# Optimization experiments

Measured on AMD Instinct MI355X. Metric: run time of the kernel, lower is better.

## Reference

```python
import jax, jax.numpy as jnp
import numpy as np

B, N, E, K, DI, DO = 16, 1024, 16, 3, 32, 32


def setup_inputs() -> dict:
    key = jax.random.key(0)
    k1, k2, k3, k4, k5 = jax.random.split(key, 5)
    return {
        "x": jax.random.normal(k1, (B, N, DI), dtype=jnp.float32),
        "all_emb": jax.random.normal(k2, (B, N, E), dtype=jnp.float32),
        "stock_emb": jax.random.normal(k3, (B, N, E), dtype=jnp.float32),
        "weights_pool": jax.random.normal(k4, (E, K, DI, DO), dtype=jnp.float32) * 0.1,
        "bias_pool": jax.random.normal(k5, (E, DO), dtype=jnp.float32) * 0.1,
    }


def reference(x, all_emb, stock_emb, weights_pool, bias_pool):
    # dynamic adjacency: relu(E E^T) then row softmax -> [B, N, N]
    A = jax.nn.relu(jnp.einsum('bne,bme->bnm', all_emb, all_emb))
    S = jax.nn.softmax(A, axis=-1)
    b, n, _ = S.shape
    k_orders = weights_pool.shape[1]
    eye = jnp.broadcast_to(jnp.eye(n, dtype=S.dtype), S.shape)
    # Chebyshev recursion T_0 = I, T_1 = S, T_k = 2 S T_{k-1} - T_{k-2}
    supports = [eye, S]
    for _ in range(2, k_orders):
        supports.append(2.0 * jnp.matmul(S, supports[-1]) - supports[-2])
    cheby = jnp.stack(supports, axis=1)  # [B, K, N, N]
    # graph propagation per Chebyshev order: [B, K, N, dim_in]
    x_g = jnp.einsum('bkij,bjd->bkid', cheby, x)
    # node-specific weights from stock_emb, fused with conv (avoids [B,N,K,I,O]):
    # original: weights = einsum('bni,ikop->bnkop'); out = einsum('bkni,bnkio->bnko').sum(k)
    out = jnp.einsum('bkni,bne,ekio->bno', x_g, stock_emb, weights_pool)
    bias = jnp.einsum('bne,eo->bno', stock_emb, bias_pool)
    return out + bias
```

## Files before the change

kernel.cpp:

```cpp
#include <hip/hip_runtime.h>
#include <stdint.h>

typedef __bf16 bf16x8 __attribute__((ext_vector_type(8)));
typedef __bf16 bf16x4 __attribute__((ext_vector_type(4)));
typedef float  f32x16 __attribute__((ext_vector_type(16)));

constexpr int kB = 16;
constexpr int kN = 1024;

struct bfhl { __bf16 h, l; };
__device__ __forceinline__ bfhl hilo(float v) {
    bfhl r;
    r.h = (__bf16)v;
    r.l = (__bf16)(v - (float)r.h);
    return r;
}

__device__ __forceinline__ int moff(int f, int h, int j) {
    return 16 * f + ((j < 4) ? (4 * h + j) : (4 * h + j + 4));
}


__global__ __launch_bounds__(256) void prep(
    const float* __restrict__ emb, const float* __restrict__ x,
    const float* __restrict__ Wp,
    __bf16* __restrict__ esf, __bf16* __restrict__ vtf1,
    __bf16* __restrict__ xgf, __bf16* __restrict__ wq)
{
    __shared__ float ls[64 * 36];
    const int tid = threadIdx.x;
    const int bid = blockIdx.x;

    if (bid < 256) {
        const int b = bid >> 4, rg = (bid & 15) << 6;
        const int r = tid >> 2, seg = tid & 3;
        float4 v = *(const float4*)(emb + ((size_t)(b * kN + rg + r) * 16 + seg * 4));
        float f[4] = {v.x, v.y, v.z, v.w};
        bf16x4 hi, lo;
        #pragma unroll
        for (int i = 0; i < 4; ++i) { bfhl t = hilo(f[i]); hi[i] = t.h; lo[i] = t.l; }
        const int kt = ((bid & 15) << 1) + (r >> 5);
        const int lane = ((seg >> 1) << 5) + (r & 31);
        const int j0 = (seg & 1) << 2;
        __bf16* base = esf + ((size_t)(b * 32 + kt) * 2) * 512 + lane * 8 + j0;
        *(bf16x4*)base         = hi;
        *(bf16x4*)(base + 512) = lo;
    } else if (bid < 512) {
        const int bb = bid - 256;
        const int b = bb >> 4, n0 = (bb & 15) << 6;
        const float* sB = x + ((size_t)b * kN + n0) * 32;
        #pragma unroll
        for (int it = 0; it < 2; ++it) {
            int f = it * 256 + tid;
            int row = f >> 3, q8 = f & 7;
            float4 v = *(const float4*)(sB + (size_t)row * 32 + q8 * 4);
            *(float4*)(&ls[row * 36 + q8 * 4]) = v;
        }
        __syncthreads();
        {
            const int mt = tid >> 7, fr = (tid >> 6) & 1, l = tid & 63;
            const int d = l & 31, h = l >> 5;
            bf16x8 ov;
            #pragma unroll
            for (int j = 0; j < 8; ++j)
                ov[j] = (__bf16)ls[(mt * 32 + moff(fr, h, j)) * 36 + d];
            *(bf16x8*)(vtf1 + ((size_t)(b * 32 + (n0 >> 5) + mt) * 2 + fr) * 512 + l * 8) = ov;
        }
        #pragma unroll
        for (int mt = 0; mt < 2; ++mt) {
            const int ks = tid >> 7, pl = (tid >> 6) & 1, l = tid & 63;
            const int node = l & 31, h = l >> 5;
            const float* rp = &ls[(mt * 32 + node) * 36 + ks * 16 + 8 * h];
            float4 u0 = *(const float4*)rp;
            float4 u1 = *(const float4*)(rp + 4);
            float u[8] = {u0.x, u0.y, u0.z, u0.w, u1.x, u1.y, u1.z, u1.w};
            bf16x8 ov;
            #pragma unroll
            for (int j = 0; j < 8; ++j) {
                bfhl t = hilo(u[j]);
                ov[j] = pl ? t.l : t.h;
            }
            const int ntile = b * 32 + (n0 >> 5) + mt;
            *(bf16x8*)(xgf + ((size_t)(ntile * 4 + ks) * 2 + pl) * 512 + l * 8) = ov;
        }
    } else {
        int idx = (bid - 512) * 256 + tid;
        if (idx < 6144) {
            int e = idx / 384, rem = idx - e * 384;
            int ks = rem / 64, r2 = rem - ks * 64;
            int o = r2 >> 1, h = r2 & 1;
            int ki0 = ks * 16 + h * 8;
            bf16x8 hi;
            #pragma unroll
            for (int j = 0; j < 8; ++j)
                hi[j] = (__bf16)Wp[(size_t)e * 3072 + (size_t)(ki0 + j) * 32 + o];
            *(bf16x8*)(wq + (size_t)(e * 6 + ks) * 512 + o * 16 + h * 8) = hi;
        }
    }
}

template<int STAGE>
__global__ __launch_bounds__(256, 2) void apply_mfma(
    const __bf16* __restrict__ esf,
    const __bf16* __restrict__ vtin,
    const float*  __restrict__ x,
    __bf16* __restrict__ vtout,
    __bf16* __restrict__ xgf,
    const __bf16* __restrict__ wq,
    const float*  __restrict__ stock,
    const float*  __restrict__ bias,
    float* __restrict__ out)
{
    __shared__ alignas(16) char smem[24576];
    float*  ps  = (float*)smem;
    float*  Ls  = (float*)(smem + 16896);
    float*  yb  = (float*)(smem + 17408);
    __bf16* xg2 = (__bf16*)(smem + 17408);
    float*  s_s = (float*)(smem + 22016);

    const int tid = threadIdx.x;
    const int w = tid >> 6, l = tid & 63;
    const int q = l & 31, h = l >> 5;
    const int b = blockIdx.x >> 5, q0 = (blockIdx.x & 31) << 5;
    const int ntile = blockIdx.x;

    const __bf16* esfB = esf + (size_t)b * 32768;
    const __bf16* vtfB = vtin + (size_t)b * 32768;

    if (STAGE == 2) {
        int r = tid >> 3, e2 = (tid & 7) * 2;
        *(float2*)(s_s + r * 16 + e2) =
            *(const float2*)(stock + (size_t)(b * kN + q0 + r) * 16 + e2);
    }

    bf16x8 bhi = *(const bf16x8*)(esfB + ((size_t)(q0 >> 5) * 2) * 512 + l * 8);
    bf16x8 blo = *(const bf16x8*)(esfB + ((size_t)(q0 >> 5) * 2 + 1) * 512 + l * 8);

    f32x16 acc = {};
    float Lp = 0.f;

    #pragma unroll 2
    for (int it = 0; it < 8; ++it) {
        const int kt = it * 4 + w;
        bf16x8 ahi = *(const bf16x8*)(esfB + ((size_t)kt * 2) * 512 + l * 8);
        bf16x8 alo = *(const bf16x8*)(esfB + ((size_t)kt * 2 + 1) * 512 + l * 8);
        bf16x8 A0  = *(const bf16x8*)(vtfB + ((size_t)kt * 2) * 512 + l * 8);
        bf16x8 A1  = *(const bf16x8*)(vtfB + ((size_t)kt * 2 + 1) * 512 + l * 8);

        f32x16 S = {};
        S = __builtin_amdgcn_mfma_f32_32x32x16_bf16(ahi, bhi, S, 0, 0, 0);
        S = __builtin_amdgcn_mfma_f32_32x32x16_bf16(ahi, blo, S, 0, 0, 0);
        S = __builtin_amdgcn_mfma_f32_32x32x16_bf16(alo, bhi, S, 0, 0, 0);

        float p[16];
        #pragma unroll
        for (int r = 0; r < 16; ++r) {
            p[r] = __expf(fmaxf(S[r], 0.f));
            Lp += p[r];
        }
        bf16x8 P0, P1;
        #pragma unroll
        for (int j = 0; j < 8; ++j) { P0[j] = (__bf16)p[j]; P1[j] = (__bf16)p[8 + j]; }

        acc = __builtin_amdgcn_mfma_f32_32x32x16_bf16(A0, P0, acc, 0, 0, 0);
        acc = __builtin_amdgcn_mfma_f32_32x32x16_bf16(A1, P1, acc, 0, 0, 0);
    }

    Lp += __shfl_xor(Lp, 32);
    #pragma unroll
    for (int r = 0; r < 16; ++r) {
        int d = (r & 3) + 8 * (r >> 2) + 4 * h;
        ps[w * 1056 + d * 33 + q] = acc[r];
    }
    if (l < 32) Ls[w * 32 + l] = Lp;
    __syncthreads();

    const int qq = tid >> 3, dg = tid & 7;
    const float iL = 1.f / (Ls[qq] + Ls[32 + qq] + Ls[64 + qq] + Ls[96 + qq]);
    float yv[4];
    #pragma unroll
    for (int i = 0; i < 4; ++i) {
        int d = dg * 4 + i;
        yv[i] = (ps[d * 33 + qq] + ps[1056 + d * 33 + qq] +
                 ps[2112 + d * 33 + qq] + ps[3168 + d * 33 + qq]) * iL;
    }

    if (STAGE == 1) {
        #pragma unroll
        for (int i = 0; i < 4; ++i) yb[qq * 36 + dg * 4 + i] = yv[i];
        __syncthreads();
        if (tid < 128) {
            const int fr = tid >> 6, l2 = tid & 63;
            const int d = l2 & 31, h2 = l2 >> 5;
            bf16x8 ov;
            #pragma unroll
            for (int j = 0; j < 8; ++j)
                ov[j] = (__bf16)yb[moff(fr, h2, j) * 36 + d];
            *(bf16x8*)(vtout + ((size_t)(b * 32 + (q0 >> 5)) * 2 + fr) * 512 + l2 * 8) = ov;
        }
        {
            const int ks2 = tid >> 7, pl = (tid >> 6) & 1, l2 = tid & 63;
            const int node = l2 & 31, h2 = l2 >> 5;
            const float* rp = &yb[node * 36 + ks2 * 16 + 8 * h2];
            float4 u0 = *(const float4*)rp;
            float4 u1 = *(const float4*)(rp + 4);
            float u[8] = {u0.x, u0.y, u0.z, u0.w, u1.x, u1.y, u1.z, u1.w};
            bf16x8 ov;
            #pragma unroll
            for (int j = 0; j < 8; ++j) {
                bfhl t = hilo(u[j]);
                ov[j] = pl ? t.l : t.h;
            }
            *(bf16x8*)(xgf + ((size_t)(ntile * 4 + 2 + ks2) * 2 + pl) * 512 + l2 * 8) = ov;
        }
    } else {
        {
            float4 xv = *(const float4*)(x + (size_t)(b * kN + q0 + qq) * 32 + dg * 4);
            float g[4] = {2.f * yv[0] - xv.x, 2.f * yv[1] - xv.y,
                          2.f * yv[2] - xv.z, 2.f * yv[3] - xv.w};
            bf16x4 hi, lo;
            #pragma unroll
            for (int i = 0; i < 4; ++i) { bfhl t = hilo(g[i]); hi[i] = t.h; lo[i] = t.l; }
            *(bf16x4*)(xg2 + qq * 36 + dg * 4)        = hi;
            *(bf16x4*)(xg2 + 1152 + qq * 36 + dg * 4) = lo;
        }
        __syncthreads();

        f32x16 acc2[4] = {};
        const int e0 = w * 4;
        const int o = q;

        #pragma unroll
        for (int ks = 0; ks < 6; ++ks) {
            bf16x8 Ah, Al;
            if (ks < 4) {
                Ah = *(const bf16x8*)(xgf + ((size_t)(ntile * 4 + ks) * 2) * 512 + l * 8);
                Al = *(const bf16x8*)(xgf + ((size_t)(ntile * 4 + ks) * 2 + 1) * 512 + l * 8);
            } else {
                const int base = o * 36 + (ks - 4) * 16 + 8 * h;
                bf16x4 a0 = *(const bf16x4*)(xg2 + base);
                bf16x4 a1 = *(const bf16x4*)(xg2 + base + 4);
                bf16x4 b0 = *(const bf16x4*)(xg2 + 1152 + base);
                bf16x4 b1 = *(const bf16x4*)(xg2 + 1152 + base + 4);
                #pragma unroll
                for (int j = 0; j < 4; ++j) {
                    Ah[j] = a0[j]; Ah[4 + j] = a1[j];
                    Al[j] = b0[j]; Al[4 + j] = b1[j];
                }
            }
            #pragma unroll
            for (int ei = 0; ei < 4; ++ei) {
                bf16x8 Bh = *(const bf16x8*)(wq + (size_t)((e0 + ei) * 6 + ks) * 512 + o * 16 + h * 8);
                acc2[ei] = __builtin_amdgcn_mfma_f32_32x32x16_bf16(Ah, Bh, acc2[ei], 0, 0, 0);
                acc2[ei] = __builtin_amdgcn_mfma_f32_32x32x16_bf16(Al, Bh, acc2[ei], 0, 0, 0);
            }
        }

        float pr[16];
        #pragma unroll
        for (int r = 0; r < 16; ++r) pr[r] = 0.f;
        #pragma unroll
        for (int ei = 0; ei < 4; ++ei) {
            const int eg = e0 + ei;
            const float bv = bias[eg * 32 + o];
            #pragma unroll
            for (int r = 0; r < 16; ++r) {
                int node = (r & 3) + 8 * (r >> 2) + 4 * h;
                pr[r] += s_s[node * 16 + eg] * (acc2[ei][r] + bv);
            }
        }
        #pragma unroll
        for (int r = 0; r < 16; ++r) {
            int node = (r & 3) + 8 * (r >> 2) + 4 * h;
            ps[w * 1056 + node * 33 + o] = pr[r];
        }
        __syncthreads();
        {
            const int node = tid >> 3, og = (tid & 7) * 4;
            float4 s;
            #pragma unroll
            for (int i = 0; i < 4; ++i) {
                int c = node * 33 + og + i;
                ((float*)&s)[i] = ps[c] + ps[1056 + c] + ps[2112 + c] + ps[3168 + c];
            }
            *(float4*)(out + (size_t)(b * kN + q0 + node) * 32 + og) = s;
        }
    }
}

extern "C" void kernel_launch(void* const* d_in, const int* in_sizes, int n_in,
                              void* d_out, int out_size, void* d_ws, size_t ws_size,
                              hipStream_t stream) {
    const float* x     = (const float*)d_in[0];
    const float* aemb  = (const float*)d_in[1];
    const float* stock = (const float*)d_in[2];
    const float* Wp    = (const float*)d_in[3];
    const float* bias  = (const float*)d_in[4];
    float* out = (float*)d_out;

    __bf16* wsb  = (__bf16*)d_ws;
    __bf16* esf  = wsb;
    __bf16* vtf1 = wsb + 524288;
    __bf16* vtf2 = wsb + 1048576;
    __bf16* xgf  = wsb + 1572864;
    __bf16* wq   = wsb + 3670016;

    prep<<<dim3(536), dim3(256), 0, stream>>>(aemb, x, Wp, esf, vtf1, xgf, wq);
    apply_mfma<1><<<dim3(512), dim3(256), 0, stream>>>(
        esf, vtf1, x, vtf2, xgf, wq, stock, bias, out);
    apply_mfma<2><<<dim3(512), dim3(256), 0, stream>>>(
        esf, vtf2, x, nullptr, xgf, wq, stock, bias, out);
}
```

Baseline: 29.10 us.

## Prefetch K tiles, fold log2e into embeddings, swizzle blocks, drop x staging

The main loop now prefetches the next two key tiles while computing the current pair, and processes two S tiles at a time for more MFMA overlap. A second embedding copy is pre-scaled by log2(e), so the softmax can use exp2f instead of __expf. Block indices are swizzled across batches. The x hi/lo split buffer is removed: stage 2 reads x directly and splits it in registers. The cost is extra register pressure and a larger prep write of the scaled embeddings, and the swizzle may change L2 locality.

```diff
diff --git a/kernel.cpp b/kernel.cpp
--- a/kernel.cpp
+++ b/kernel.cpp
@@ -7,6 +7,7 @@
 
 constexpr int kB = 16;
 constexpr int kN = 1024;
+constexpr float kLog2e = 1.44269504088896340736f;
 
 struct bfhl { __bf16 h, l; };
 __device__ __forceinline__ bfhl hilo(float v) {
@@ -24,8 +25,8 @@
 __global__ __launch_bounds__(256) void prep(
     const float* __restrict__ emb, const float* __restrict__ x,
     const float* __restrict__ Wp,
-    __bf16* __restrict__ esf, __bf16* __restrict__ vtf1,
-    __bf16* __restrict__ xgf, __bf16* __restrict__ wq)
+    __bf16* __restrict__ esf, __bf16* __restrict__ esq,
+    __bf16* __restrict__ vtf1, __bf16* __restrict__ wq)
 {
     __shared__ float ls[64 * 36];
     const int tid = threadIdx.x;
@@ -36,15 +37,20 @@
         const int r = tid >> 2, seg = tid & 3;
         float4 v = *(const float4*)(emb + ((size_t)(b * kN + rg + r) * 16 + seg * 4));
         float f[4] = {v.x, v.y, v.z, v.w};
-        bf16x4 hi, lo;
-        #pragma unroll
-        for (int i = 0; i < 4; ++i) { bfhl t = hilo(f[i]); hi[i] = t.h; lo[i] = t.l; }
+        bf16x4 hi, lo, qhi, qlo;
+        #pragma unroll
+        for (int i = 0; i < 4; ++i) {
+            bfhl t = hilo(f[i]);           hi[i] = t.h;  lo[i] = t.l;
+            bfhl s = hilo(f[i] * kLog2e);  qhi[i] = s.h; qlo[i] = s.l;
+        }
         const int kt = ((bid & 15) << 1) + (r >> 5);
         const int lane = ((seg >> 1) << 5) + (r & 31);
         const int j0 = (seg & 1) << 2;
-        __bf16* base = esf + ((size_t)(b * 32 + kt) * 2) * 512 + lane * 8 + j0;
-        *(bf16x4*)base         = hi;
-        *(bf16x4*)(base + 512) = lo;
+        const size_t off = ((size_t)(b * 32 + kt) * 2) * 512 + lane * 8 + j0;
+        *(bf16x4*)(esf + off)       = hi;
+        *(bf16x4*)(esf + off + 512) = lo;
+        *(bf16x4*)(esq + off)       = qhi;
+        *(bf16x4*)(esq + off + 512) = qlo;
     } else if (bid < 512) {
         const int bb = bid - 256;
         const int b = bb >> 4, n0 = (bb & 15) << 6;
@@ -66,65 +72,48 @@
                 ov[j] = (__bf16)ls[(mt * 32 + moff(fr, h, j)) * 36 + d];
             *(bf16x8*)(vtf1 + ((size_t)(b * 32 + (n0 >> 5) + mt) * 2 + fr) * 512 + l * 8) = ov;
         }
-        #pragma unroll
-        for (int mt = 0; mt < 2; ++mt) {
-            const int ks = tid >> 7, pl = (tid >> 6) & 1, l = tid & 63;
-            const int node = l & 31, h = l >> 5;
-            const float* rp = &ls[(mt * 32 + node) * 36 + ks * 16 + 8 * h];
-            float4 u0 = *(const float4*)rp;
-            float4 u1 = *(const float4*)(rp + 4);
-            float u[8] = {u0.x, u0.y, u0.z, u0.w, u1.x, u1.y, u1.z, u1.w};
-            bf16x8 ov;
-            #pragma unroll
-            for (int j = 0; j < 8; ++j) {
-                bfhl t = hilo(u[j]);
-                ov[j] = pl ? t.l : t.h;
-            }
-            const int ntile = b * 32 + (n0 >> 5) + mt;
-            *(bf16x8*)(xgf + ((size_t)(ntile * 4 + ks) * 2 + pl) * 512 + l * 8) = ov;
-        }
     } else {
         int idx = (bid - 512) * 256 + tid;
         if (idx < 6144) {
             int e = idx / 384, rem = idx - e * 384;
             int ks = rem / 64, r2 = rem - ks * 64;
-            int o = r2 >> 1, h = r2 & 1;
-            int ki0 = ks * 16 + h * 8;
+            int o = r2 >> 1, hh = r2 & 1;
+            int ki0 = ks * 16 + hh * 8;
             bf16x8 hi;
             #pragma unroll
             for (int j = 0; j < 8; ++j)
                 hi[j] = (__bf16)Wp[(size_t)e * 3072 + (size_t)(ki0 + j) * 32 + o];
-            *(bf16x8*)(wq + (size_t)(e * 6 + ks) * 512 + o * 16 + h * 8) = hi;
+            *(bf16x8*)(wq + (size_t)(e * 6 + ks) * 512 + o * 16 + hh * 8) = hi;
         }
     }
 }
 
 template<int STAGE>
 __global__ __launch_bounds__(256, 2) void apply_mfma(
-    const __bf16* __restrict__ esf,
+    const __bf16* __restrict__ esf, const __bf16* __restrict__ esq,
     const __bf16* __restrict__ vtin,
     const float*  __restrict__ x,
-    __bf16* __restrict__ vtout,
-    __bf16* __restrict__ xgf,
+    __bf16* __restrict__ vtout, __bf16* __restrict__ y1f,
     const __bf16* __restrict__ wq,
-    const float*  __restrict__ stock,
-    const float*  __restrict__ bias,
+    const float*  __restrict__ stock, const float* __restrict__ bias,
     float* __restrict__ out)
 {
-    __shared__ alignas(16) char smem[24576];
+    __shared__ alignas(16) char smem[28672];
     float*  ps  = (float*)smem;
     float*  Ls  = (float*)(smem + 16896);
     float*  yb  = (float*)(smem + 17408);
-    __bf16* xg2 = (__bf16*)(smem + 17408);
-    float*  s_s = (float*)(smem + 22016);
+    __bf16* xg2 = (__bf16*)(smem + 22016);
+    float*  s_s = (float*)(smem + 26624);
 
     const int tid = threadIdx.x;
     const int w = tid >> 6, l = tid & 63;
     const int q = l & 31, h = l >> 5;
-    const int b = blockIdx.x >> 5, q0 = (blockIdx.x & 31) << 5;
-    const int ntile = blockIdx.x;
+    const int bs = ((blockIdx.x & 7) << 6) | (blockIdx.x >> 3);
+    const int b = bs >> 5, nt = bs & 31, q0 = nt << 5;
+    const int gnt = b * 32 + nt;
 
     const __bf16* esfB = esf + (size_t)b * 32768;
+    const __bf16* esqB = esq + (size_t)b * 32768;
     const __bf16* vtfB = vtin + (size_t)b * 32768;
 
     if (STAGE == 2) {
@@ -133,38 +122,59 @@
             *(const float2*)(stock + (size_t)(b * kN + q0 + r) * 16 + e2);
     }
 
-    bf16x8 bhi = *(const bf16x8*)(esfB + ((size_t)(q0 >> 5) * 2) * 512 + l * 8);
-    bf16x8 blo = *(const bf16x8*)(esfB + ((size_t)(q0 >> 5) * 2 + 1) * 512 + l * 8);
+    bf16x8 bhi = *(const bf16x8*)(esqB + ((size_t)nt * 2) * 512 + l * 8);
+    bf16x8 blo = *(const bf16x8*)(esqB + ((size_t)nt * 2 + 1) * 512 + l * 8);
 
     f32x16 acc = {};
     float Lp = 0.f;
 
-    #pragma unroll 2
-    for (int it = 0; it < 8; ++it) {
-        const int kt = it * 4 + w;
-        bf16x8 ahi = *(const bf16x8*)(esfB + ((size_t)kt * 2) * 512 + l * 8);
-        bf16x8 alo = *(const bf16x8*)(esfB + ((size_t)kt * 2 + 1) * 512 + l * 8);
-        bf16x8 A0  = *(const bf16x8*)(vtfB + ((size_t)kt * 2) * 512 + l * 8);
-        bf16x8 A1  = *(const bf16x8*)(vtfB + ((size_t)kt * 2 + 1) * 512 + l * 8);
-
-        f32x16 S = {};
-        S = __builtin_amdgcn_mfma_f32_32x32x16_bf16(ahi, bhi, S, 0, 0, 0);
-        S = __builtin_amdgcn_mfma_f32_32x32x16_bf16(ahi, blo, S, 0, 0, 0);
-        S = __builtin_amdgcn_mfma_f32_32x32x16_bf16(alo, bhi, S, 0, 0, 0);
-
-        float p[16];
+#define LOADK(kt, ahi, alo, V0, V1) \
+    ahi = *(const bf16x8*)(esfB + ((size_t)(kt) * 2) * 512 + l * 8);     \
+    alo = *(const bf16x8*)(esfB + ((size_t)(kt) * 2 + 1) * 512 + l * 8); \
+    V0  = *(const bf16x8*)(vtfB + ((size_t)(kt) * 2) * 512 + l * 8);     \
+    V1  = *(const bf16x8*)(vtfB + ((size_t)(kt) * 2 + 1) * 512 + l * 8);
+
+    const int ktb = w * 8;
+    bf16x8 cahiA, caloA, cV0A, cV1A, cahiB, caloB, cV0B, cV1B;
+    LOADK(ktb + 0, cahiA, caloA, cV0A, cV1A);
+    LOADK(ktb + 1, cahiB, caloB, cV0B, cV1B);
+
+    #pragma unroll
+    for (int it = 0; it < 4; ++it) {
+        bf16x8 nahiA, naloA, nV0A, nV1A, nahiB, naloB, nV0B, nV1B;
+        if (it < 3) {
+            LOADK(ktb + it * 2 + 2, nahiA, naloA, nV0A, nV1A);
+            LOADK(ktb + it * 2 + 3, nahiB, naloB, nV0B, nV1B);
+        }
+        f32x16 S0 = {}, S1 = {};
+        S0 = __builtin_amdgcn_mfma_f32_32x32x16_bf16(cahiA, bhi, S0, 0, 0, 0);
+        S1 = __builtin_amdgcn_mfma_f32_32x32x16_bf16(cahiB, bhi, S1, 0, 0, 0);
+        S0 = __builtin_amdgcn_mfma_f32_32x32x16_bf16(cahiA, blo, S0, 0, 0, 0);
+        S1 = __builtin_amdgcn_mfma_f32_32x32x16_bf16(cahiB, blo, S1, 0, 0, 0);
+        S0 = __builtin_amdgcn_mfma_f32_32x32x16_bf16(caloA, bhi, S0, 0, 0, 0);
+        S1 = __builtin_amdgcn_mfma_f32_32x32x16_bf16(caloB, bhi, S1, 0, 0, 0);
+
+        float p0[16], p1[16];
         #pragma unroll
         for (int r = 0; r < 16; ++r) {
-            p[r] = __expf(fmaxf(S[r], 0.f));
-            Lp += p[r];
-        }
-        bf16x8 P0, P1;
-        #pragma unroll
-        for (int j = 0; j < 8; ++j) { P0[j] = (__bf16)p[j]; P1[j] = (__bf16)p[8 + j]; }
-
-        acc = __builtin_amdgcn_mfma_f32_32x32x16_bf16(A0, P0, acc, 0, 0, 0);
-        acc = __builtin_amdgcn_mfma_f32_32x32x16_bf16(A1, P1, acc, 0, 0, 0);
-    }
+            p0[r] = exp2f(fmaxf(S0[r], 0.f));  Lp += p0[r];
+            p1[r] = exp2f(fmaxf(S1[r], 0.f));  Lp += p1[r];
+        }
+        bf16x8 P00, P01, P10, P11;
+        #pragma unroll
+        for (int j = 0; j < 8; ++j) {
+            P00[j] = (__bf16)p0[j]; P01[j] = (__bf16)p0[8 + j];
+            P10[j] = (__bf16)p1[j]; P11[j] = (__bf16)p1[8 + j];
+        }
+        acc = __builtin_amdgcn_mfma_f32_32x32x16_bf16(cV0A, P00, acc, 0, 0, 0);
+        acc = __builtin_amdgcn_mfma_f32_32x32x16_bf16(cV1A, P01, acc, 0, 0, 0);
+        acc = __builtin_amdgcn_mfma_f32_32x32x16_bf16(cV0B, P10, acc, 0, 0, 0);
+        acc = __builtin_amdgcn_mfma_f32_32x32x16_bf16(cV1B, P11, acc, 0, 0, 0);
+
+        cahiA = nahiA; caloA = naloA; cV0A = nV0A; cV1A = nV1A;
+        cahiB = nahiB; caloB = naloB; cV0B = nV0B; cV1B = nV1B;
+    }
+#undef LOADK
 
     Lp += __shfl_xor(Lp, 32);
     #pragma unroll
@@ -190,37 +200,36 @@
         for (int i = 0; i < 4; ++i) yb[qq * 36 + dg * 4 + i] = yv[i];
         __syncthreads();
         if (tid < 128) {
-            const int fr = tid >> 6, l2 = tid & 63;
-            const int d = l2 & 31, h2 = l2 >> 5;
+            int fr = tid >> 6, l2 = tid & 63;
+            int d = l2 & 31, h2 = l2 >> 5;
             bf16x8 ov;
             #pragma unroll
             for (int j = 0; j < 8; ++j)
                 ov[j] = (__bf16)yb[moff(fr, h2, j) * 36 + d];
-            *(bf16x8*)(vtout + ((size_t)(b * 32 + (q0 >> 5)) * 2 + fr) * 512 + l2 * 8) = ov;
+            *(bf16x8*)(vtout + ((size_t)gnt * 2 + fr) * 512 + l2 * 8) = ov;
         }
         {
-            const int ks2 = tid >> 7, pl = (tid >> 6) & 1, l2 = tid & 63;
-            const int node = l2 & 31, h2 = l2 >> 5;
-            const float* rp = &yb[node * 36 + ks2 * 16 + 8 * h2];
-            float4 u0 = *(const float4*)rp;
-            float4 u1 = *(const float4*)(rp + 4);
-            float u[8] = {u0.x, u0.y, u0.z, u0.w, u1.x, u1.y, u1.z, u1.w};
+            int ks2 = tid >> 7, pl = (tid >> 6) & 1, l2 = tid & 63;
+            int node = l2 & 31, h2 = l2 >> 5;
+            const float* rp = yb + node * 36 + ks2 * 16 + 8 * h2;
             bf16x8 ov;
             #pragma unroll
             for (int j = 0; j < 8; ++j) {
-                bfhl t = hilo(u[j]);
-                ov[j] = pl ? t.l : t.h;
-            }
-            *(bf16x8*)(xgf + ((size_t)(ntile * 4 + 2 + ks2) * 2 + pl) * 512 + l2 * 8) = ov;
+                bfhl tt = hilo(rp[j]);
+                ov[j] = pl ? tt.l : tt.h;
+            }
+            *(bf16x8*)(y1f + (((size_t)gnt * 2 + ks2) * 2 + pl) * 512 + l2 * 8) = ov;
         }
     } else {
         {
             float4 xv = *(const float4*)(x + (size_t)(b * kN + q0 + qq) * 32 + dg * 4);
-            float g[4] = {2.f * yv[0] - xv.x, 2.f * yv[1] - xv.y,
-                          2.f * yv[2] - xv.z, 2.f * yv[3] - xv.w};
+            float xa[4] = {xv.x, xv.y, xv.z, xv.w};
             bf16x4 hi, lo;
             #pragma unroll
-            for (int i = 0; i < 4; ++i) { bfhl t = hilo(g[i]); hi[i] = t.h; lo[i] = t.l; }
+            for (int i = 0; i < 4; ++i) {
+                bfhl tt = hilo(2.f * yv[i] - xa[i]);
+                hi[i] = tt.h; lo[i] = tt.l;
+            }
             *(bf16x4*)(xg2 + qq * 36 + dg * 4)        = hi;
             *(bf16x4*)(xg2 + 1152 + qq * 36 + dg * 4) = lo;
         }
@@ -233,9 +242,16 @@
         #pragma unroll
         for (int ks = 0; ks < 6; ++ks) {
             bf16x8 Ah, Al;
-            if (ks < 4) {
-                Ah = *(const bf16x8*)(xgf + ((size_t)(ntile * 4 + ks) * 2) * 512 + l * 8);
-                Al = *(const bf16x8*)(xgf + ((size_t)(ntile * 4 + ks) * 2 + 1) * 512 + l * 8);
+            if (ks < 2) {
+                const float* rp = x + (size_t)(b * kN + q0 + q) * 32 + ks * 16 + 8 * h;
+                float4 u0 = *(const float4*)rp;
+                float4 u1 = *(const float4*)(rp + 4);
+                float u[8] = {u0.x, u0.y, u0.z, u0.w, u1.x, u1.y, u1.z, u1.w};
+                #pragma unroll
+                for (int j = 0; j < 8; ++j) { bfhl tt = hilo(u[j]); Ah[j] = tt.h; Al[j] = tt.l; }
+            } else if (ks < 4) {
+                Ah = *(const bf16x8*)(y1f + (((size_t)gnt * 2 + (ks - 2)) * 2 + 0) * 512 + l * 8);
+                Al = *(const bf16x8*)(y1f + (((size_t)gnt * 2 + (ks - 2)) * 2 + 1) * 512 + l * 8);
             } else {
                 const int base = o * 36 + (ks - 4) * 16 + 8 * h;
                 bf16x4 a0 = *(const bf16x4*)(xg2 + base);
@@ -300,14 +316,15 @@
 
     __bf16* wsb  = (__bf16*)d_ws;
     __bf16* esf  = wsb;
-    __bf16* vtf1 = wsb + 524288;
-    __bf16* vtf2 = wsb + 1048576;
-    __bf16* xgf  = wsb + 1572864;
-    __bf16* wq   = wsb + 3670016;
-
-    prep<<<dim3(536), dim3(256), 0, stream>>>(aemb, x, Wp, esf, vtf1, xgf, wq);
+    __bf16* esq  = wsb + 524288;
+    __bf16* vtf1 = wsb + 1048576;
+    __bf16* vtf2 = wsb + 1572864;
+    __bf16* y1f  = wsb + 2097152;
+    __bf16* wq   = wsb + 3145728;
+
+    prep<<<dim3(536), dim3(256), 0, stream>>>(aemb, x, Wp, esf, esq, vtf1, wq);
     apply_mfma<1><<<dim3(512), dim3(256), 0, stream>>>(
-        esf, vtf1, x, vtf2, xgf, wq, stock, bias, out);
+        esf, esq, vtf1, x, vtf2, y1f, wq, stock, bias, out);
     apply_mfma<2><<<dim3(512), dim3(256), 0, stream>>>(
-        esf, vtf2, x, nullptr, xgf, wq, stock, bias, out);
-}
+        esf, esq, vtf2, x, nullptr, y1f, wq, stock, bias, out);
+}
```

Result: no change. 28.95 us (-0.5%).
